# Optimization experiments

Measured on AMD Instinct MI355X. Metric: run time of the kernel, lower is better.

The kernel has to match this reference:

```python
import jax, jax.numpy as jnp
import numpy as np

G = 16          # grid_size
B = 2           # num graphs
SPACING = 1.5   # anchor_spacing
KA = 8          # atom_k_neighbors
KG = 24         # k_neighbors (grid->atom)
CUTOFF = 8.0
T = 16          # n_atom_types
H = 240         # hidden irreps dim (64x0e+32x1o+16x2e)
A = 9           # SH attr dim, lmax=2
C = 32          # code_dim
L = 2           # num_layers
BIG = 1e9

# real spherical harmonics, 'integral' normalization, e3nn component order
C0 = 0.28209479177387814   # 1/(2 sqrt(pi))
C1 = 0.4886025119029199    # sqrt(3/(4 pi))
C2A = 1.0925484305920792   # sqrt(15/(4 pi))
C2B = 0.31539156525252005  # sqrt(5/(16 pi))
C2C = 0.5462742152960396   # sqrt(15/(16 pi))

def _sph(rel, dist):
    u = rel / jnp.maximum(dist, 1e-9)[:, None]
    x, y, z = u[:, 0], u[:, 1], u[:, 2]
    return jnp.stack([
        jnp.full_like(x, C0),
        C1 * y, C1 * z, C1 * x,
        C2A * x * y, C2A * y * z, C2B * (3.0 * z * z - 1.0),
        C2A * z * x, C2C * (x * x - y * y),
    ], axis=-1)


def setup_inputs():
    key = jax.random.key(0)
    ks = jax.random.split(key, 12)
    Na = 1024
    half = G * SPACING / 2.0
    pos = jax.random.uniform(ks[0], (Na, 3), minval=-half, maxval=half, dtype=jnp.float32)
    atom_types = jax.random.randint(ks[1], (Na,), 0, T, dtype=jnp.int32)
    atom_batch = jnp.repeat(jnp.arange(B, dtype=jnp.int32), Na // B)

    def lin(k, shape):
        fan_in = shape[-2]
        return jax.random.normal(k, shape, dtype=jnp.float32) / jnp.sqrt(float(fan_in))

    Din = 2 * H + A
    return dict(
        pos=pos, atom_types=atom_types, atom_batch=atom_batch,
        We=lin(ks[2], (T + A, H)), be=jnp.zeros((H,), jnp.float32),
        Wm1=lin(ks[3], (L, Din, H)), bm1=jnp.zeros((L, H), jnp.float32),
        Wm2=lin(ks[4], (L, H, H)), bm2=jnp.zeros((L, H), jnp.float32),
        Wu1=lin(ks[5], (L, Din, H)), bu1=jnp.zeros((L, H), jnp.float32),
        Wu2=lin(ks[6], (L, H, H)), bu2=jnp.zeros((L, H), jnp.float32),
        Wo1=lin(ks[7], (H, H)), bo1=jnp.zeros((H,), jnp.float32),
        Wo2=lin(ks[8], (H, C)), bo2=jnp.zeros((C,), jnp.float32),
    )


def _forward(pos, atom_types, atom_batch, We, be, Wm1, bm1, Wm2, bm2,
             Wu1, bu1, Wu2, bu2, Wo1, bo1, Wo2, bo2):
    Na = pos.shape[0]
    ng = G ** 3
    Ng = B * ng
    N = Na + Ng

    # anchor grid, centered, spacing SPACING
    ax = (jnp.arange(G, dtype=pos.dtype) - (G - 1) / 2.0) * SPACING
    grid = jnp.stack(jnp.meshgrid(ax, ax, ax, indexing='ij'), -1).reshape(-1, 3)  # [ng,3]
    grid_flat = jnp.tile(grid, (B, 1))                                            # [Ng,3]
    grid_batch = jnp.repeat(jnp.arange(B, dtype=atom_batch.dtype), ng)
    node_pos = jnp.concatenate([pos, grid_flat], 0)                               # [N,3]

    # atom-atom knn_graph (no self loops, per-graph)
    d2 = jnp.sum((pos[:, None] - pos[None]) ** 2, -1)                             # [Na,Na]
    d2 = jnp.where(atom_batch[:, None] == atom_batch[None], d2, BIG)
    d2 = jnp.where(jnp.eye(Na, dtype=bool), BIG, d2)
    _, nbr = jax.lax.top_k(-d2, KA)                                               # [Na,KA]

    # grid->atom knn (per-graph), edge src=atom, dst=grid node
    d2g = jnp.sum((grid_flat[:, None] - pos[None]) ** 2, -1)                      # [Ng,Na]
    d2g = jnp.where(grid_batch[:, None] == atom_batch[None], d2g, BIG)
    _, nbg = jax.lax.top_k(-d2g, KG)                                              # [Ng,KG]

    src = jnp.concatenate([nbr.reshape(-1), nbg.reshape(-1)])
    dst = jnp.concatenate([jnp.repeat(jnp.arange(Na), KA),
                           Na + jnp.repeat(jnp.arange(Ng), KG)])

    rel = node_pos[src] - node_pos[dst]
    dist = jnp.linalg.norm(rel, axis=-1)
    mask = (dist <= CUTOFF).astype(pos.dtype)        # cutoff as mask (jit-friendly)
    ea = _sph(rel, dist) * mask[:, None]             # [E,A]

    # node attrs: scatter-mean of edge SH over destination nodes
    na_sum = jax.ops.segment_sum(ea, dst, num_segments=N)
    cnt = jax.ops.segment_sum(mask, dst, num_segments=N)
    node_attr = na_sum / jnp.maximum(cnt, 1.0)[:, None]
    node_attr = node_attr.at[:, 0].set(1.0)

    # node features: one-hot atoms, zeros for anchors
    feat = jnp.concatenate([jax.nn.one_hot(atom_types, T, dtype=pos.dtype),
                            jnp.zeros((Ng, T), pos.dtype)], 0)
    h = jax.nn.silu(jnp.concatenate([feat, node_attr], -1) @ We + be)

    # SEGNN-style message passing (attr-conditioned MLPs, masked-sum aggregation)
    for l in range(L):
        mi = jnp.concatenate([h[src], h[dst], ea], -1)                            # [E,2H+A]
        m = jax.nn.silu(jax.nn.silu(mi @ Wm1[l] + bm1[l]) @ Wm2[l] + bm2[l])
        m = m * mask[:, None]
        agg = jax.ops.segment_sum(m, dst, num_segments=N)                         # [N,H]
        ui = jnp.concatenate([h, agg, node_attr], -1)                             # [N,2H+A]
        h = h + jax.nn.silu(jax.nn.silu(ui @ Wu1[l] + bu1[l]) @ Wu2[l] + bu2[l])

    out = jax.nn.silu(h @ Wo1 + bo1) @ Wo2 + bo2                                  # [N,C]
    return out[Na:].reshape(B, ng, C)


def reference(pos, atom_types, atom_batch, We, be, Wm1, bm1, Wm2, bm2,
              Wu1, bu1, Wu2, bu2, Wo1, bo1, Wo2, bo2):
    return _forward(pos, atom_types, atom_batch, We, be, Wm1, bm1, Wm2, bm2,
                    Wu1, bu1, Wu2, bu2, Wo1, bo1, Wo2, bo2)
```

## Files before the change

### kernel.cpp

```cpp
#include <hip/hip_runtime.h>
#include <math.h>

#define NA   1024
#define NGRID 4096
#define NB   2
#define NG   (NB*NGRID)
#define NN   (NA+NG)
#define KAK  8
#define KGK  24
#define EAE  (NA*KAK)
#define EGE  (NG*KGK)
#define ET   (EAE+EGE)
#define HD   240
#define TT   16
#define DIN  489
#define CD   32
#define CUTF 8.0f

typedef __attribute__((ext_vector_type(8))) short short8;
typedef __attribute__((ext_vector_type(4))) short short4v;
typedef __attribute__((ext_vector_type(4))) float f32x4;
typedef __attribute__((ext_vector_type(4))) int i32x4;

__device__ __forceinline__ float silu_f(float x) {
    return x / (1.0f + __expf(-x));
}
__device__ __forceinline__ short f2bf(float x) {
    unsigned u = __float_as_uint(x);
    unsigned r = (u + 0x7FFFu + ((u >> 16) & 1u)) >> 16;
    return (short)r;
}
__device__ __forceinline__ float bf2f(short s) {
    return __uint_as_float(((unsigned)(unsigned short)s) << 16);
}
__device__ __forceinline__ unsigned cvt_pk_bf16(float lo, float hi) {
    unsigned r;
    asm("v_cvt_pk_bf16_f32 %0, %1, %2" : "=v"(r) : "v"(lo), "v"(hi));
    return r;
}

template <int K>
__device__ __forceinline__ void wave_topk(unsigned long long key[8], int lane,
                                          int* __restrict__ outp) {
    unsigned long long lmin = key[0];
#pragma unroll
    for (int s = 1; s < 8; ++s) lmin = key[s] < lmin ? key[s] : lmin;
    int myout = -1;
    for (int t = 0; t < K; ++t) {
        unsigned long long m = lmin;
#pragma unroll
        for (int d = 1; d < 64; d <<= 1) {
            unsigned long long o = __shfl_xor(m, d);
            m = o < m ? o : m;
        }
        if (lane == t) myout = (int)(m & 1023u);
        if (m == lmin) {
#pragma unroll
            for (int s = 0; s < 8; ++s) if (key[s] == m) key[s] = ~0ull;
            lmin = key[0];
#pragma unroll
            for (int s = 1; s < 8; ++s) lmin = key[s] < lmin ? key[s] : lmin;
        }
    }
    if (lane < K) outp[lane] = myout;
}

__global__ __launch_bounds__(256) void knn_kernel(const float* __restrict__ pos,
                                                  int* __restrict__ nbr,
                                                  int* __restrict__ nbg) {
    __shared__ float sx[512], sy[512], sz[512];
    int tid = threadIdx.x;
    bool isAtom = blockIdx.x < (NA / 4);
    int q0 = isAtom ? blockIdx.x * 4 : (blockIdx.x - NA / 4) * 4;
    int pbase;
    if (isAtom) pbase = (q0 >= 512) ? 512 : 0;
    else        pbase = (q0 >= NGRID) ? 512 : 0;
    for (int j = tid; j < 512; j += 256) {
        sx[j] = pos[(pbase + j)*3 + 0];
        sy[j] = pos[(pbase + j)*3 + 1];
        sz[j] = pos[(pbase + j)*3 + 2];
    }
    __syncthreads();
    int lane = tid & 63;
    int qq = q0 + (tid >> 6);
    if (isAtom) {
        int i = qq;
        float px = sx[i - pbase], py = sy[i - pbase], pz = sz[i - pbase];
        unsigned long long key[8];
#pragma unroll
        for (int s = 0; s < 8; ++s) {
            int c = s * 64 + lane;
            int j = pbase + c;
            float dx = px - sx[c], dy = py - sy[c], dz = pz - sz[c];
            float d2 = __fadd_rn(__fadd_rn(__fmul_rn(dx,dx), __fmul_rn(dy,dy)), __fmul_rn(dz,dz));
            key[s] = ((unsigned long long)__float_as_uint(d2) << 10) | (unsigned)j;
            if (j == i) key[s] = ~0ull;
        }
        wave_topk<KAK>(key, lane, &nbr[i*KAK]);
    } else {
        int g = qq;
        int gi = g & (NGRID - 1);
        int ix = gi >> 8, iy = (gi >> 4) & 15, iz = gi & 15;
        float px = ((float)ix - 7.5f) * 1.5f;
        float py = ((float)iy - 7.5f) * 1.5f;
        float pz = ((float)iz - 7.5f) * 1.5f;
        unsigned long long key[8];
#pragma unroll
        for (int s = 0; s < 8; ++s) {
            int c = s * 64 + lane;
            int j = pbase + c;
            float dx = px - sx[c], dy = py - sy[c], dz = pz - sz[c];
            float d2 = __fadd_rn(__fadd_rn(__fmul_rn(dx,dx), __fmul_rn(dy,dy)), __fmul_rn(dz,dz));
            key[s] = ((unsigned long long)__float_as_uint(d2) << 10) | (unsigned)j;
        }
        wave_topk<KGK>(key, lane, &nbg[g*KGK]);
    }
}

__global__ void edge_kernel(const float* __restrict__ pos, const int* __restrict__ nbr,
                            const int* __restrict__ nbg, float* __restrict__ ea,
                            float* __restrict__ emask) {
    int e = blockIdx.x * blockDim.x + threadIdx.x;
    if (e >= ET) return;
    int src; float dpx, dpy, dpz;
    if (e < EAE) {
        int d = e >> 3;
        src = nbr[e];
        dpx = pos[d*3]; dpy = pos[d*3+1]; dpz = pos[d*3+2];
    } else {
        int eg = e - EAE;
        src = nbg[eg];
        int gg = eg / KGK;
        int gi = gg % NGRID;
        int ix = gi >> 8, iy = (gi >> 4) & 15, iz = gi & 15;
        dpx = ((float)ix - 7.5f) * 1.5f;
        dpy = ((float)iy - 7.5f) * 1.5f;
        dpz = ((float)iz - 7.5f) * 1.5f;
    }
    float rx = pos[src*3] - dpx, ry = pos[src*3+1] - dpy, rz = pos[src*3+2] - dpz;
    float dist = sqrtf(rx*rx + ry*ry + rz*rz);
    float mask = (dist <= CUTF) ? 1.0f : 0.0f;
    float inv = 1.0f / fmaxf(dist, 1e-9f);
    float x = rx * inv, y = ry * inv, z = rz * inv;
    float s0 = 0.28209479177387814f;
    float s1 = 0.4886025119029199f * y;
    float s2 = 0.4886025119029199f * z;
    float s3 = 0.4886025119029199f * x;
    float s4 = 1.0925484305920792f * x * y;
    float s5 = 1.0925484305920792f * y * z;
    float s6 = 0.31539156525252005f * (3.0f * z * z - 1.0f);
    float s7 = 1.0925484305920792f * z * x;
    float s8 = 0.5462742152960396f * (x * x - y * y);
    float* o = &ea[(size_t)e * 9];
    o[0] = s0 * mask; o[1] = s1 * mask; o[2] = s2 * mask; o[3] = s3 * mask;
    o[4] = s4 * mask; o[5] = s5 * mask; o[6] = s6 * mask; o[7] = s7 * mask; o[8] = s8 * mask;
    emask[e] = mask;
}

__global__ void node_attr_kernel(const float* __restrict__ ea, const float* __restrict__ emask,
                                 float* __restrict__ attr) {
    int n = blockIdx.x * blockDim.x + threadIdx.x;
    if (n >= NN) return;
    int K, e0;
    if (n < NA) { K = KAK; e0 = n * KAK; }
    else        { K = KGK; e0 = EAE + (n - NA) * KGK; }
    float s[9];
#pragma unroll
    for (int a = 0; a < 9; ++a) s[a] = 0.f;
    float cnt = 0.f;
    for (int k = 0; k < K; ++k) {
        cnt += emask[e0 + k];
        const float* p = &ea[(size_t)(e0 + k) * 9];
#pragma unroll
        for (int a = 0; a < 9; ++a) s[a] += p[a];
    }
    float invc = 1.0f / fmaxf(cnt, 1.0f);
    attr[n*9+0] = 1.0f;
#pragma unroll
    for (int a = 1; a < 9; ++a) attr[n*9+a] = s[a] * invc;
}

__global__ void encoder_kernel(const int* __restrict__ types, const float* __restrict__ attr,
                               const float* __restrict__ We, const float* __restrict__ be,
                               float* __restrict__ h) {
    int idx = blockIdx.x * blockDim.x + threadIdx.x;
    int n = idx / HD, j = idx % HD;
    float acc = be[j];
    if (n < NA) acc += We[types[n] * HD + j];
#pragma unroll
    for (int a = 0; a < 9; ++a) acc += attr[n*9+a] * We[(TT + a) * HD + j];
    h[idx] = silu_f(acc);
}

__global__ void convert_all_kernel(const float* __restrict__ Wm2, const float* __restrict__ Wu1,
                                   const float* __restrict__ Wu2, const float* __restrict__ Wm1,
                                   short* __restrict__ wm2t, short* __restrict__ wu1t,
                                   short* __restrict__ wu2t,
                                   short* __restrict__ wzd_hi, short* __restrict__ wzd_lo,
                                   short* __restrict__ wzs_hi, short* __restrict__ wzs_lo) {
    int idx = blockIdx.x * blockDim.x + threadIdx.x;
    if (idx < 131072) {
        int l = idx >> 16, rem = idx & 65535, col = rem >> 8, k = rem & 255;
        short v = 0;
        if (k < 240 && col < 240) v = f2bf(Wm2[(size_t)l*57600 + k*240 + col]);
        wm2t[idx] = v;
    } else if (idx < 393216) {
        int i = idx - 131072;
        int l = i / 131072, rem = i % 131072, col = rem >> 9, k = rem & 511;
        short v = 0;
        if (k < DIN && col < 240) v = f2bf(Wu1[(size_t)l*DIN*240 + (size_t)k*240 + col]);
        wu1t[i] = v;
    } else if (idx < 524288) {
        int i = idx - 393216;
        int l = i >> 16, rem = i & 65535, col = rem >> 8, k = rem & 255;
        short v = 0;
        if (k < 240 && col < 240) v = f2bf(Wu2[(size_t)l*57600 + k*240 + col]);
        wu2t[i] = v;
    } else if (idx < 655360) {
        int i = idx - 524288;
        int l = i >> 16, rem = i & 65535, col = rem >> 8, k = rem & 255;
        float v = 0.f;
        if (k < 240 && col < 240) v = Wm1[(size_t)l*DIN*HD + (size_t)(240 + k)*HD + col];
        short hh = f2bf(v);
        wzd_hi[i] = hh;
        wzd_lo[i] = f2bf(v - bf2f(hh));
    } else {
        int i = idx - 655360;
        int l = i >> 16, rem = i & 65535, col = rem >> 8, k = rem & 255;
        float v = 0.f;
        if (k < 240 && col < 240) v = Wm1[(size_t)l*DIN*HD + (size_t)k*HD + col];
        short hh = f2bf(v);
        wzs_hi[i] = hh;
        wzs_lo[i] = f2bf(v - bf2f(hh));
    }
}

__global__ __launch_bounds__(256) void node_z_mfma_kernel(
        const float* __restrict__ h,
        const short* __restrict__ wzd_hi, const short* __restrict__ wzd_lo,
        const short* __restrict__ wzs_hi, const short* __restrict__ wzs_lo,
        const float* __restrict__ bm1,
        float* __restrict__ Zs, float* __restrict__ Zd) {
    __shared__ __align__(16) short Ahi[32 * 256];
    __shared__ __align__(16) short Alo[32 * 256];
    int tid = threadIdx.x;
    int n0 = blockIdx.x * 32;

#pragma unroll
    for (int it = 0; it < 4; ++it) {
        int idx = it * 256 + tid;
        int row = idx >> 5, q = idx & 31;
        int j = q * 8;
        short8 ohi = {0,0,0,0,0,0,0,0}, olo = {0,0,0,0,0,0,0,0};
        if (j < 240) {
            const float4 a0 = *(const float4*)(h + (size_t)(n0 + row) * HD + j);
            const float4 a1 = *(const float4*)(h + (size_t)(n0 + row) * HD + j + 4);
            float v[8] = {a0.x, a0.y, a0.z, a0.w, a1.x, a1.y, a1.z, a1.w};
#pragma unroll
            for (int a = 0; a < 8; ++a) {
                short hh = f2bf(v[a]);
                ohi[a] = hh;
                olo[a] = f2bf(v[a] - bf2f(hh));
            }
        }
        int boff = row * 512 + ((q * 16) ^ ((row & 7) << 4));
        *(short8*)((char*)Ahi + boff) = ohi;
        *(short8*)((char*)Alo + boff) = olo;
    }
    __syncthreads();

    int wid = tid >> 6, lane = tid & 63;
    int mw = wid >> 1, nw = wid & 1;
    int lg = lane >> 4, lc = lane & 15;
    int col0 = nw * 128;
    int arow = (mw * 16 + lc) * 256;

    f32x4 acc[8];
#pragma unroll
    for (int nt = 0; nt < 8; ++nt) acc[nt] = (f32x4){0.f, 0.f, 0.f, 0.f};
#pragma unroll
    for (int kc = 0; kc < 8; ++kc) {
        int aoff = arow + ((kc * 32 + lg * 8) ^ ((lc & 7) << 3));
        const short8 ahi = *(const short8*)&Ahi[aoff];
        const short8 alo = *(const short8*)&Alo[aoff];
#pragma unroll
        for (int nt = 0; nt < 8; ++nt) {
            size_t bo = (size_t)(col0 + nt*16 + lc) * 256 + kc*32 + lg*8;
            const short8 bhi = *(const short8*)(wzd_hi + bo);
            const short8 blo = *(const short8*)(wzd_lo + bo);
            acc[nt] = __builtin_amdgcn_mfma_f32_16x16x32_bf16(ahi, bhi, acc[nt], 0, 0, 0);
            acc[nt] = __builtin_amdgcn_mfma_f32_16x16x32_bf16(ahi, blo, acc[nt], 0, 0, 0);
            acc[nt] = __builtin_amdgcn_mfma_f32_16x16x32_bf16(alo, bhi, acc[nt], 0, 0, 0);
        }
    }
#pragma unroll
    for (int nt = 0; nt < 8; ++nt) {
        int ncol = col0 + nt * 16 + lc;
        if (ncol < HD) {
            float bias = bm1[ncol];
            float vals[4] = {acc[nt].x, acc[nt].y, acc[nt].z, acc[nt].w};
#pragma unroll
            for (int r = 0; r < 4; ++r)
                Zd[(size_t)(n0 + mw*16 + lg*4 + r) * HD + ncol] = vals[r] + bias;
        }
    }

    if (n0 < NA) {
#pragma unroll
        for (int nt = 0; nt < 8; ++nt) acc[nt] = (f32x4){0.f, 0.f, 0.f, 0.f};
#pragma unroll
        for (int kc = 0; kc < 8; ++kc) {
            int aoff = arow + ((kc * 32 + lg * 8) ^ ((lc & 7) << 3));
            const short8 ahi = *(const short8*)&Ahi[aoff];
            const short8 alo = *(const short8*)&Alo[aoff];
#pragma unroll
            for (int nt = 0; nt < 8; ++nt) {
                size_t bo = (size_t)(col0 + nt*16 + lc) * 256 + kc*32 + lg*8;
                const short8 bhi = *(const short8*)(wzs_hi + bo);
                const short8 blo = *(const short8*)(wzs_lo + bo);
                acc[nt] = __builtin_amdgcn_mfma_f32_16x16x32_bf16(ahi, bhi, acc[nt], 0, 0, 0);
                acc[nt] = __builtin_amdgcn_mfma_f32_16x16x32_bf16(ahi, blo, acc[nt], 0, 0, 0);
                acc[nt] = __builtin_amdgcn_mfma_f32_16x16x32_bf16(alo, bhi, acc[nt], 0, 0, 0);
            }
        }
#pragma unroll
        for (int nt = 0; nt < 8; ++nt) {
            int ncol = col0 + nt * 16 + lc;
            if (ncol < HD) {
                float vals[4] = {acc[nt].x, acc[nt].y, acc[nt].z, acc[nt].w};
#pragma unroll
                for (int r = 0; r < 4; ++r)
                    Zs[(size_t)(n0 + mw*16 + lg*4 + r) * HD + ncol] = vals[r];
            }
        }
    }
}

__global__ __launch_bounds__(256) void msg_gemm_kernel(
        const float* __restrict__ Zs, const float* __restrict__ Zd,
        const int* __restrict__ nbg, const float* __restrict__ ea,
        const float* __restrict__ emask, const float* __restrict__ Wea,
        const short* __restrict__ wm2t, const float* __restrict__ bm2,
        float* __restrict__ agg) {
    __shared__ __align__(16) short Abuf[48 * 256];
    __shared__ __align__(16) float mkbuf[48];
    int tid = threadIdx.x;
    int blk = blockIdx.x;
    int e0 = blk * 48;

    int q = tid & 31;
    int rh = tid >> 5;
    float4 w0[9], w1[9];
    float4 zdA0, zdA1, zdB0, zdB1;
    int srcs[6];
    if (q < 30) {
        int j = q * 8;
#pragma unroll
        for (int a = 0; a < 9; ++a) {
            w0[a] = *(const float4*)(Wea + a * HD + j);
            w1[a] = *(const float4*)(Wea + a * HD + j + 4);
        }
#pragma unroll
        for (int r8 = 0; r8 < 6; ++r8) srcs[r8] = nbg[e0 + rh + r8 * 8];
        int dn0 = NA + blk * 2;
        zdA0 = *(const float4*)(Zd + (size_t)dn0 * HD + j);
        zdA1 = *(const float4*)(Zd + (size_t)dn0 * HD + j + 4);
        zdB0 = *(const float4*)(Zd + (size_t)(dn0 + 1) * HD + j);
        zdB1 = *(const float4*)(Zd + (size_t)(dn0 + 1) * HD + j + 4);
    }
    if (tid < 48) mkbuf[tid] = emask[EAE + e0 + tid];

#pragma unroll
    for (int r8 = 0; r8 < 6; ++r8) {
        int row = rh + r8 * 8;
        i32x4 oi = (i32x4){0, 0, 0, 0};
        if (q < 30) {
            int j = q * 8;
            int eg = e0 + row;
            int srcn = srcs[r8];
            const float4 zs0 = *(const float4*)(Zs + (size_t)srcn * HD + j);
            const float4 zs1 = *(const float4*)(Zs + (size_t)srcn * HD + j + 4);
            const float4 zd0 = (r8 < 3) ? zdA0 : zdB0;
            const float4 zd1 = (r8 < 3) ? zdA1 : zdB1;
            float s0 = zs0.x + zd0.x, s1 = zs0.y + zd0.y, s2 = zs0.z + zd0.z, s3 = zs0.w + zd0.w;
            float s4 = zs1.x + zd1.x, s5 = zs1.y + zd1.y, s6 = zs1.z + zd1.z, s7 = zs1.w + zd1.w;
            const float* ep = ea + (size_t)(EAE + eg) * 9;
#pragma unroll
            for (int a = 0; a < 9; ++a) {
                float e = ep[a];
                s0 += e * w0[a].x; s1 += e * w0[a].y; s2 += e * w0[a].z; s3 += e * w0[a].w;
                s4 += e * w1[a].x; s5 += e * w1[a].y; s6 += e * w1[a].z; s7 += e * w1[a].w;
            }
            oi[0] = (int)cvt_pk_bf16(silu_f(s0), silu_f(s1));
            oi[1] = (int)cvt_pk_bf16(silu_f(s2), silu_f(s3));
            oi[2] = (int)cvt_pk_bf16(silu_f(s4), silu_f(s5));
            oi[3] = (int)cvt_pk_bf16(silu_f(s6), silu_f(s7));
        }
        *(i32x4*)((char*)Abuf + row * 512 + ((q * 16) ^ ((row & 7) << 4))) = oi;
    }
    __syncthreads();

    int wid = tid >> 6, lane = tid & 63;
    int lg = lane >> 4, lc = lane & 15;
    int col0 = wid * 64;

    f32x4 acc[3][4];
#pragma unroll
    for (int mt = 0; mt < 3; ++mt)
#pragma unroll
        for (int nt = 0; nt < 4; ++nt) acc[mt][nt] = (f32x4){0.f, 0.f, 0.f, 0.f};

#pragma unroll
    for (int kc = 0; kc < 8; ++kc) {
        short8 af[3];
#pragma unroll
        for (int mt = 0; mt < 3; ++mt)
            af[mt] = *(const short8*)&Abuf[(mt*16 + lc) * 256 +
                                           ((kc*32 + lg*8) ^ ((lc & 7) << 3))];
#pragma unroll
        for (int nt = 0; nt < 4; ++nt) {
            const short8 bf = *(const short8*)(wm2t + (size_t)(col0 + nt*16 + lc) * 256 + kc*32 + lg*8);
#pragma unroll
            for (int mt = 0; mt < 3; ++mt)
                acc[mt][nt] = __builtin_amdgcn_mfma_f32_16x16x32_bf16(af[mt], bf, acc[mt][nt], 0, 0, 0);
        }
    }

#pragma unroll
    for (int nt = 0; nt < 4; ++nt) {
        int ncol = col0 + nt * 16 + lc;
        float bias = (ncol < HD) ? bm2[ncol] : 0.f;
        float p[3];
#pragma unroll
        for (int mt = 0; mt < 3; ++mt) {
            const float4 mkv = *(const float4*)&mkbuf[mt*16 + lg*4];
            float t0 = silu_f(acc[mt][nt].x + bias) * mkv.x;
            float t1 = silu_f(acc[mt][nt].y + bias) * mkv.y;
            float t2 = silu_f(acc[mt][nt].z + bias) * mkv.z;
            float t3 = silu_f(acc[mt][nt].w + bias) * mkv.w;
            p[mt] = (t0 + t1) + (t2 + t3);
        }
        float v0 = p[0] + ((lg < 2) ? p[1] : 0.f);
        float v1 = ((lg >= 2) ? p[1] : 0.f) + p[2];
        v0 += __shfl_xor(v0, 16); v0 += __shfl_xor(v0, 32);
        v1 += __shfl_xor(v1, 16); v1 += __shfl_xor(v1, 32);
        if (ncol < HD) {
            int node = NA + blk * 2;
            if (lane < 16)      agg[(size_t)(node + 0) * HD + ncol] = v0;
            else if (lane < 32) agg[(size_t)(node + 1) * HD + ncol] = v1;
        }
    }
}

template <int KE, int NPB>
__global__ __launch_bounds__(192) void msg_mfma_kernel(
        const float* __restrict__ Zs, const float* __restrict__ Zd,
        const int* __restrict__ nbrList, const float* __restrict__ ea,
        const float* __restrict__ emask, const float* __restrict__ Wea,
        const short* __restrict__ wm2t, const float* __restrict__ bm2,
        float* __restrict__ agg, int dstBase, int edgeBase) {
    constexpr int ROWS = KE * NPB;
    constexpr int MT = ROWS / 16;
    __shared__ __align__(16) short Abuf[ROWS * 264];
    __shared__ __align__(16) float mkbuf[ROWS];

    int tid = threadIdx.x;
    int b = blockIdx.x;
    int e0 = edgeBase + b * ROWS;

    if (tid < ROWS) mkbuf[tid] = emask[e0 + tid];
    for (int idx = tid; idx < ROWS * 24; idx += 192) {
        int r = idx / 24;
        Abuf[r * 264 + 240 + (idx % 24)] = 0;
    }
    for (int idx = tid; idx < ROWS * 60; idx += 192) {
        int row = idx / 60;
        int j = (idx % 60) * 4;
        int srcn = nbrList[b * ROWS + row];
        int dstn = dstBase + b * NPB + row / KE;
        const float4 zs = *(const float4*)(Zs + (size_t)srcn * HD + j);
        const float4 zd = *(const float4*)(Zd + (size_t)dstn * HD + j);
        float s0 = zs.x + zd.x, s1 = zs.y + zd.y, s2 = zs.z + zd.z, s3 = zs.w + zd.w;
        const float* ep = ea + (size_t)(e0 + row) * 9;
#pragma unroll
        for (int a = 0; a < 9; ++a) {
            float ev = ep[a];
            const float4 w = *(const float4*)(Wea + a * HD + j);
            s0 += ev * w.x; s1 += ev * w.y; s2 += ev * w.z; s3 += ev * w.w;
        }
        short4v o;
        o.x = f2bf(silu_f(s0)); o.y = f2bf(silu_f(s1));
        o.z = f2bf(silu_f(s2)); o.w = f2bf(silu_f(s3));
        *(short4v*)&Abuf[row * 264 + j] = o;
    }
    __syncthreads();

    int w = tid / 64, lane = tid % 64;
    int lg = lane >> 4, lc = lane & 15;
    int wcol0 = w * 80;

    f32x4 acc[MT][5];
#pragma unroll
    for (int mt = 0; mt < MT; ++mt)
#pragma unroll
        for (int nt = 0; nt < 5; ++nt) acc[mt][nt] = (f32x4){0.f, 0.f, 0.f, 0.f};

#pragma unroll
    for (int kc = 0; kc < 8; ++kc) {
        short8 af[MT];
#pragma unroll
        for (int mt = 0; mt < MT; ++mt)
            af[mt] = *(const short8*)&Abuf[(mt * 16 + lc) * 264 + kc * 32 + lg * 8];
#pragma unroll
        for (int nt = 0; nt < 5; ++nt) {
            const short8 bf = *(const short8*)(wm2t + (size_t)(wcol0 + nt * 16 + lc) * 256 + kc * 32 + lg * 8);
#pragma unroll
            for (int mt = 0; mt < MT; ++mt)
                acc[mt][nt] = __builtin_amdgcn_mfma_f32_16x16x32_bf16(af[mt], bf, acc[mt][nt], 0, 0, 0);
        }
    }

#pragma unroll
    for (int nt = 0; nt < 5; ++nt) {
        int ncol = wcol0 + nt * 16 + lc;
        float bias = bm2[ncol];
        float p[MT];
#pragma unroll
        for (int mt = 0; mt < MT; ++mt) {
            const float4 mkv = *(const float4*)&mkbuf[mt * 16 + lg * 4];
            float t0 = silu_f(acc[mt][nt].x + bias) * mkv.x;
            float t1 = silu_f(acc[mt][nt].y + bias) * mkv.y;
            float t2 = silu_f(acc[mt][nt].z + bias) * mkv.z;
            float t3 = silu_f(acc[mt][nt].w + bias) * mkv.w;
            p[mt] = (t0 + t1) + (t2 + t3);
        }
#pragma unroll
        for (int mt = 0; mt < MT; ++mt) {
            float v = p[mt];
            v += __shfl_xor(v, 16);
            if (lane < 16)
                agg[(size_t)(dstBase + b * (2 * MT) + 2 * mt + 0) * HD + ncol] = v;
            else if (lane >= 32 && lane < 48)
                agg[(size_t)(dstBase + b * (2 * MT) + 2 * mt + 1) * HD + ncol] = v;
        }
    }
}

__global__ __launch_bounds__(256) void update_mfma_kernel(
        float* __restrict__ h, const float* __restrict__ agg,
        const float* __restrict__ attr,
        const short* __restrict__ wu1t, const float* __restrict__ bu1,
        const short* __restrict__ wu2t, const float* __restrict__ bu2) {
    __shared__ __align__(16) short Abuf[32 * 512];
    __shared__ __align__(16) short Ubuf[32 * 256];
    int tid = threadIdx.x;
    int n0 = blockIdx.x * 32;

#pragma unroll
    for (int it = 0; it < 8; ++it) {
        int idx = it * 256 + tid;
        int row = idx >> 6, q = idx & 63;
        int j = q * 8;
        int n = n0 + row;
        short8 o = {0,0,0,0,0,0,0,0};
        if (j < 240) {
            const float4 a0 = *(const float4*)(h + (size_t)n * HD + j);
            const float4 a1 = *(const float4*)(h + (size_t)n * HD + j + 4);
            o[0]=f2bf(a0.x); o[1]=f2bf(a0.y); o[2]=f2bf(a0.z); o[3]=f2bf(a0.w);
            o[4]=f2bf(a1.x); o[5]=f2bf(a1.y); o[6]=f2bf(a1.z); o[7]=f2bf(a1.w);
        } else if (j < 480) {
            const float4 a0 = *(const float4*)(agg + (size_t)n * HD + (j - 240));
            const float4 a1 = *(const float4*)(agg + (size_t)n * HD + (j - 240) + 4);
            o[0]=f2bf(a0.x); o[1]=f2bf(a0.y); o[2]=f2bf(a0.z); o[3]=f2bf(a0.w);
            o[4]=f2bf(a1.x); o[5]=f2bf(a1.y); o[6]=f2bf(a1.z); o[7]=f2bf(a1.w);
        } else if (j == 480) {
#pragma unroll
            for (int a = 0; a < 8; ++a) o[a] = f2bf(attr[n*9 + a]);
        } else if (j == 488) {
            o[0] = f2bf(attr[n*9 + 8]);
        }
        *(short8*)((char*)Abuf + row * 1024 + ((q * 16) ^ ((row & 7) << 4))) = o;
    }
    __syncthreads();

    int wid = tid >> 6, lane = tid & 63;
    int mw = wid >> 1, nw = wid & 1;
    int lg = lane >> 4, lc = lane & 15;
    int col0 = nw * 128;

    f32x4 acc[8];
#pragma unroll
    for (int nt = 0; nt < 8; ++nt) acc[nt] = (f32x4){0.f, 0.f, 0.f, 0.f};
#pragma unroll
    for (int kc = 0; kc < 16; ++kc) {
        const short8 af = *(const short8*)((char*)Abuf + (mw*16 + lc) * 1024 +
                                           ((kc*64 + lg*16) ^ ((lc & 7) << 4)));
#pragma unroll
        for (int nt = 0; nt < 8; ++nt) {
            const short8 bf = *(const short8*)(wu1t + (size_t)(col0 + nt*16 + lc) * 512 + kc*32 + lg*8);
            acc[nt] = __builtin_amdgcn_mfma_f32_16x16x32_bf16(af, bf, acc[nt], 0, 0, 0);
        }
    }
#pragma unroll
    for (int nt = 0; nt < 8; ++nt) {
        int ncol = col0 + nt * 16 + lc;
        float bias = (ncol < HD) ? bu1[ncol] : 0.f;
        float vals[4] = {acc[nt].x, acc[nt].y, acc[nt].z, acc[nt].w};
#pragma unroll
        for (int r = 0; r < 4; ++r) {
            int row = mw*16 + lg*4 + r;
            *(short*)((char*)Ubuf + row * 512 + ((ncol * 2) ^ ((row & 7) << 4))) =
                f2bf(silu_f(vals[r] + bias));
        }
    }
    __syncthreads();

    f32x4 acc2[8];
#pragma unroll
    for (int nt = 0; nt < 8; ++nt) acc2[nt] = (f32x4){0.f, 0.f, 0.f, 0.f};
#pragma unroll
    for (int kc = 0; kc < 8; ++kc) {
        const short8 af = *(const short8*)((char*)Ubuf + (mw*16 + lc) * 512 +
                                           ((kc*64 + lg*16) ^ ((lc & 7) << 4)));
#pragma unroll
        for (int nt = 0; nt < 8; ++nt) {
            const short8 bf = *(const short8*)(wu2t + (size_t)(col0 + nt*16 + lc) * 256 + kc*32 + lg*8);
            acc2[nt] = __builtin_amdgcn_mfma_f32_16x16x32_bf16(af, bf, acc2[nt], 0, 0, 0);
        }
    }
#pragma unroll
    for (int nt = 0; nt < 8; ++nt) {
        int ncol = col0 + nt * 16 + lc;
        if (ncol < HD) {
            float bias = bu2[ncol];
            float vals[4] = {acc2[nt].x, acc2[nt].y, acc2[nt].z, acc2[nt].w};
#pragma unroll
            for (int r = 0; r < 4; ++r) {
                int row = mw*16 + lg*4 + r;
                size_t hi = (size_t)(n0 + row) * HD + ncol;
                h[hi] += silu_f(vals[r] + bias);
            }
        }
    }
}

__global__ void output_kernel(const float* __restrict__ h,
                              const float* __restrict__ Wo1, const float* __restrict__ bo1,
                              const float* __restrict__ Wo2, const float* __restrict__ bo2,
                              float* __restrict__ out) {
    const int NBT = 4;
    __shared__ float hr[NBT][HD];
    __shared__ float o1[NBT][HD];
    int tid = threadIdx.x;
    int g0 = blockIdx.x * NBT;
    for (int idx = tid; idx < NBT * HD; idx += 256) {
        int k = idx / HD, i = idx % HD;
        hr[k][i] = h[(size_t)(NA + g0 + k) * HD + i];
    }
    __syncthreads();
    int j = tid;
    if (j < HD) {
        float acc[NBT] = {0.f, 0.f, 0.f, 0.f};
        for (int i4 = 0; i4 < 60; ++i4) {
            int i = 4 * i4;
            float w0 = Wo1[(i+0)*HD+j], w1 = Wo1[(i+1)*HD+j];
            float w2 = Wo1[(i+2)*HD+j], w3 = Wo1[(i+3)*HD+j];
#pragma unroll
            for (int k = 0; k < NBT; ++k) {
                const float4 a = *reinterpret_cast<const float4*>(&hr[k][i]);
                acc[k] += a.x*w0 + a.y*w1 + a.z*w2 + a.w*w3;
            }
        }
        float bb = bo1[j];
#pragma unroll
        for (int k = 0; k < NBT; ++k) o1[k][j] = silu_f(acc[k] + bb);
    }
    __syncthreads();
    if (tid < NBT * CD) {
        int k = tid >> 5, c = tid & 31;
        float acc = bo2[c];
        for (int i = 0; i < HD; ++i) acc += o1[k][i] * Wo2[i*CD + c];
        out[(size_t)(g0 + k) * CD + c] = acc;
    }
}

extern "C" void kernel_launch(void* const* d_in, const int* in_sizes, int n_in,
                              void* d_out, int out_size, void* d_ws, size_t ws_size,
                              hipStream_t stream) {
    (void)in_sizes; (void)n_in; (void)out_size; (void)ws_size;
    const float* pos   = (const float*)d_in[0];
    const int*   types = (const int*)d_in[1];
    const int*   batch = (const int*)d_in[2];
    (void)batch;
    const float* We    = (const float*)d_in[3];
    const float* be    = (const float*)d_in[4];
    const float* Wm1   = (const float*)d_in[5];
    const float* bm1   = (const float*)d_in[6];
    const float* Wm2   = (const float*)d_in[7];
    const float* bm2   = (const float*)d_in[8];
    const float* Wu1   = (const float*)d_in[9];
    const float* bu1   = (const float*)d_in[10];
    const float* Wu2   = (const float*)d_in[11];
    const float* bu2   = (const float*)d_in[12];
    const float* Wo1   = (const float*)d_in[13];
    const float* bo1   = (const float*)d_in[14];
    const float* Wo2   = (const float*)d_in[15];
    const float* bo2   = (const float*)d_in[16];
    float* out = (float*)d_out;

    char* ws = (char*)d_ws;
    size_t off = 0;
    auto take = [&](size_t bytes) -> char* {
        char* p = ws + off;
        off = (off + bytes + 255) & ~(size_t)255;
        return p;
    };
    int*   nbr    = (int*)take((size_t)EAE * 4);
    int*   nbg    = (int*)take((size_t)EGE * 4);
    float* ea     = (float*)take((size_t)ET * 9 * 4);
    float* emask  = (float*)take((size_t)ET * 4);
    float* attr   = (float*)take((size_t)NN * 9 * 4);
    float* h      = (float*)take((size_t)NN * HD * 4);
    float* agg    = (float*)take((size_t)NN * HD * 4);
    float* zs     = (float*)take((size_t)NA * HD * 4);
    float* zd     = (float*)take((size_t)NN * HD * 4);
    short* wm2t   = (short*)take((size_t)2 * 256 * 256 * 2);
    short* wu1t   = (short*)take((size_t)2 * 256 * 512 * 2);
    short* wu2t   = (short*)take((size_t)2 * 256 * 256 * 2);
    short* wzd_hi = (short*)take((size_t)2 * 256 * 256 * 2);
    short* wzd_lo = (short*)take((size_t)2 * 256 * 256 * 2);
    short* wzs_hi = (short*)take((size_t)2 * 256 * 256 * 2);
    short* wzs_lo = (short*)take((size_t)2 * 256 * 256 * 2);

    knn_kernel<<<NA/4 + NG/4, 256, 0, stream>>>(pos, nbr, nbg);
    edge_kernel<<<ET/256, 256, 0, stream>>>(pos, nbr, nbg, ea, emask);
    node_attr_kernel<<<NN/256, 256, 0, stream>>>(ea, emask, attr);
    encoder_kernel<<<(NN*HD)/256, 256, 0, stream>>>(types, attr, We, be, h);
    convert_all_kernel<<<786432/256, 256, 0, stream>>>(Wm2, Wu1, Wu2, Wm1,
                                                       wm2t, wu1t, wu2t,
                                                       wzd_hi, wzd_lo, wzs_hi, wzs_lo);

    for (int l = 0; l < 2; ++l) {
        const float* wm1 = Wm1 + (size_t)l * DIN * HD;
        const float* wea = wm1 + (size_t)480 * HD;
        const short* w2t = wm2t + (size_t)l * 256 * 256;
        const float* bb2 = bm2 + l * HD;
        node_z_mfma_kernel<<<NN/32, 256, 0, stream>>>(
            h,
            wzd_hi + (size_t)l * 65536, wzd_lo + (size_t)l * 65536,
            wzs_hi + (size_t)l * 65536, wzs_lo + (size_t)l * 65536,
            bm1 + l * HD, zs, zd);
        msg_mfma_kernel<KAK, 8><<<NA*KAK/64, 192, 0, stream>>>(
            zs, zd, nbr, ea, emask, wea, w2t, bb2, agg, 0, 0);
        msg_gemm_kernel<<<EGE/48, 256, 0, stream>>>(zs, zd, nbg, ea, emask, wea, w2t, bb2, agg);
        update_mfma_kernel<<<NN/32, 256, 0, stream>>>(
            h, agg, attr,
            wu1t + (size_t)l * 256 * 512, bu1 + l * HD,
            wu2t + (size_t)l * 256 * 256, bu2 + l * HD);
    }
    output_kernel<<<NG/4, 256, 0, stream>>>(h, Wo1, bo1, Wo2, bo2, out);
}
```

Before: 626.0 us.

## Split edge attributes into vector arrays and double-buffer msg_gemm over four tiles

Result: slower. 723.4 us (+15.6%).

```diff
diff --git a/kernel.cpp b/kernel.cpp
--- a/kernel.cpp
+++ b/kernel.cpp
@@ -118,7 +118,8 @@
 }
 
 __global__ void edge_kernel(const float* __restrict__ pos, const int* __restrict__ nbr,
-                            const int* __restrict__ nbg, float* __restrict__ ea,
+                            const int* __restrict__ nbg, float4* __restrict__ eaA,
+                            float4* __restrict__ eaB, float* __restrict__ eaC,
                             float* __restrict__ emask) {
     int e = blockIdx.x * blockDim.x + threadIdx.x;
     if (e >= ET) return;
@@ -151,13 +152,14 @@
     float s6 = 0.31539156525252005f * (3.0f * z * z - 1.0f);
     float s7 = 1.0925484305920792f * z * x;
     float s8 = 0.5462742152960396f * (x * x - y * y);
-    float* o = &ea[(size_t)e * 9];
-    o[0] = s0 * mask; o[1] = s1 * mask; o[2] = s2 * mask; o[3] = s3 * mask;
-    o[4] = s4 * mask; o[5] = s5 * mask; o[6] = s6 * mask; o[7] = s7 * mask; o[8] = s8 * mask;
+    eaA[e] = (float4){s0*mask, s1*mask, s2*mask, s3*mask};
+    eaB[e] = (float4){s4*mask, s5*mask, s6*mask, s7*mask};
+    eaC[e] = s8 * mask;
     emask[e] = mask;
 }
 
-__global__ void node_attr_kernel(const float* __restrict__ ea, const float* __restrict__ emask,
+__global__ void node_attr_kernel(const float4* __restrict__ eaA, const float4* __restrict__ eaB,
+                                 const float* __restrict__ eaC, const float* __restrict__ emask,
                                  float* __restrict__ attr) {
     int n = blockIdx.x * blockDim.x + threadIdx.x;
     if (n >= NN) return;
@@ -170,9 +172,11 @@
     float cnt = 0.f;
     for (int k = 0; k < K; ++k) {
         cnt += emask[e0 + k];
-        const float* p = &ea[(size_t)(e0 + k) * 9];
-#pragma unroll
-        for (int a = 0; a < 9; ++a) s[a] += p[a];
+        const float4 a0 = eaA[e0 + k];
+        const float4 a1 = eaB[e0 + k];
+        s[0] += a0.x; s[1] += a0.y; s[2] += a0.z; s[3] += a0.w;
+        s[4] += a1.x; s[5] += a1.y; s[6] += a1.z; s[7] += a1.w;
+        s[8] += eaC[e0 + k];
     }
     float invc = 1.0f / fmaxf(cnt, 1.0f);
     attr[n*9+0] = 1.0f;
@@ -338,21 +342,20 @@
 
 __global__ __launch_bounds__(256) void msg_gemm_kernel(
         const float* __restrict__ Zs, const float* __restrict__ Zd,
-        const int* __restrict__ nbg, const float* __restrict__ ea,
+        const int* __restrict__ nbg,
+        const float4* __restrict__ eaA, const float4* __restrict__ eaB,
+        const float* __restrict__ eaC,
         const float* __restrict__ emask, const float* __restrict__ Wea,
         const short* __restrict__ wm2t, const float* __restrict__ bm2,
         float* __restrict__ agg) {
-    __shared__ __align__(16) short Abuf[48 * 256];
-    __shared__ __align__(16) float mkbuf[48];
+    __shared__ __align__(16) short Abuf[2][48 * 256];
+    __shared__ __align__(16) float mkbuf[2][48];
     int tid = threadIdx.x;
-    int blk = blockIdx.x;
-    int e0 = blk * 48;
+    int blk0 = blockIdx.x * 4;
 
     int q = tid & 31;
     int rh = tid >> 5;
     float4 w0[9], w1[9];
-    float4 zdA0, zdA1, zdB0, zdB1;
-    int srcs[6];
     if (q < 30) {
         int j = q * 8;
 #pragma unroll
@@ -360,102 +363,127 @@
             w0[a] = *(const float4*)(Wea + a * HD + j);
             w1[a] = *(const float4*)(Wea + a * HD + j + 4);
         }
-#pragma unroll
-        for (int r8 = 0; r8 < 6; ++r8) srcs[r8] = nbg[e0 + rh + r8 * 8];
-        int dn0 = NA + blk * 2;
-        zdA0 = *(const float4*)(Zd + (size_t)dn0 * HD + j);
-        zdA1 = *(const float4*)(Zd + (size_t)dn0 * HD + j + 4);
-        zdB0 = *(const float4*)(Zd + (size_t)(dn0 + 1) * HD + j);
-        zdB1 = *(const float4*)(Zd + (size_t)(dn0 + 1) * HD + j + 4);
-    }
-    if (tid < 48) mkbuf[tid] = emask[EAE + e0 + tid];
-
-#pragma unroll
-    for (int r8 = 0; r8 < 6; ++r8) {
-        int row = rh + r8 * 8;
-        i32x4 oi = (i32x4){0, 0, 0, 0};
+    }
+
+    auto assemble = [&](int tile, int bufi) {
+        int e0 = tile * 48;
+        if (tid < 48) mkbuf[bufi][tid] = emask[EAE + e0 + tid];
         if (q < 30) {
             int j = q * 8;
-            int eg = e0 + row;
-            int srcn = srcs[r8];
-            const float4 zs0 = *(const float4*)(Zs + (size_t)srcn * HD + j);
-            const float4 zs1 = *(const float4*)(Zs + (size_t)srcn * HD + j + 4);
-            const float4 zd0 = (r8 < 3) ? zdA0 : zdB0;
-            const float4 zd1 = (r8 < 3) ? zdA1 : zdB1;
-            float s0 = zs0.x + zd0.x, s1 = zs0.y + zd0.y, s2 = zs0.z + zd0.z, s3 = zs0.w + zd0.w;
-            float s4 = zs1.x + zd1.x, s5 = zs1.y + zd1.y, s6 = zs1.z + zd1.z, s7 = zs1.w + zd1.w;
-            const float* ep = ea + (size_t)(EAE + eg) * 9;
-#pragma unroll
-            for (int a = 0; a < 9; ++a) {
-                float e = ep[a];
-                s0 += e * w0[a].x; s1 += e * w0[a].y; s2 += e * w0[a].z; s3 += e * w0[a].w;
-                s4 += e * w1[a].x; s5 += e * w1[a].y; s6 += e * w1[a].z; s7 += e * w1[a].w;
-            }
-            oi[0] = (int)cvt_pk_bf16(silu_f(s0), silu_f(s1));
-            oi[1] = (int)cvt_pk_bf16(silu_f(s2), silu_f(s3));
-            oi[2] = (int)cvt_pk_bf16(silu_f(s4), silu_f(s5));
-            oi[3] = (int)cvt_pk_bf16(silu_f(s6), silu_f(s7));
-        }
-        *(i32x4*)((char*)Abuf + row * 512 + ((q * 16) ^ ((row & 7) << 4))) = oi;
-    }
+            int srcs[6];
+#pragma unroll
+            for (int r8 = 0; r8 < 6; ++r8) srcs[r8] = nbg[e0 + rh + r8 * 8];
+            int dn0 = NA + tile * 2;
+            const float4 zdA0 = *(const float4*)(Zd + (size_t)dn0 * HD + j);
+            const float4 zdA1 = *(const float4*)(Zd + (size_t)dn0 * HD + j + 4);
+            const float4 zdB0 = *(const float4*)(Zd + (size_t)(dn0 + 1) * HD + j);
+            const float4 zdB1 = *(const float4*)(Zd + (size_t)(dn0 + 1) * HD + j + 4);
+#pragma unroll
+            for (int r8 = 0; r8 < 6; ++r8) {
+                int row = rh + r8 * 8;
+                int eg = e0 + row;
+                int srcn = srcs[r8];
+                const float4 zs0 = *(const float4*)(Zs + (size_t)srcn * HD + j);
+                const float4 zs1 = *(const float4*)(Zs + (size_t)srcn * HD + j + 4);
+                const float4 zd0 = (r8 < 3) ? zdA0 : zdB0;
+                const float4 zd1 = (r8 < 3) ? zdA1 : zdB1;
+                float s0 = zs0.x + zd0.x, s1 = zs0.y + zd0.y, s2 = zs0.z + zd0.z, s3 = zs0.w + zd0.w;
+                float s4 = zs1.x + zd1.x, s5 = zs1.y + zd1.y, s6 = zs1.z + zd1.z, s7 = zs1.w + zd1.w;
+                const float4 ea0 = eaA[EAE + eg];
+                const float4 ea1 = eaB[EAE + eg];
+                const float  ea8 = eaC[EAE + eg];
+                float ev[9] = {ea0.x, ea0.y, ea0.z, ea0.w, ea1.x, ea1.y, ea1.z, ea1.w, ea8};
+#pragma unroll
+                for (int a = 0; a < 9; ++a) {
+                    float e = ev[a];
+                    s0 += e * w0[a].x; s1 += e * w0[a].y; s2 += e * w0[a].z; s3 += e * w0[a].w;
+                    s4 += e * w1[a].x; s5 += e * w1[a].y; s6 += e * w1[a].z; s7 += e * w1[a].w;
+                }
+                i32x4 oi;
+                oi[0] = (int)cvt_pk_bf16(silu_f(s0), silu_f(s1));
+                oi[1] = (int)cvt_pk_bf16(silu_f(s2), silu_f(s3));
+                oi[2] = (int)cvt_pk_bf16(silu_f(s4), silu_f(s5));
+                oi[3] = (int)cvt_pk_bf16(silu_f(s6), silu_f(s7));
+                *(i32x4*)((char*)&Abuf[bufi][0] + row * 512 + ((q * 16) ^ ((row & 7) << 4))) = oi;
+            }
+        } else {
+#pragma unroll
+            for (int r8 = 0; r8 < 6; ++r8) {
+                int row = rh + r8 * 8;
+                i32x4 z = (i32x4){0, 0, 0, 0};
+                *(i32x4*)((char*)&Abuf[bufi][0] + row * 512 + ((q * 16) ^ ((row & 7) << 4))) = z;
+            }
+        }
+    };
+
+    assemble(blk0, 0);
     __syncthreads();
 
     int wid = tid >> 6, lane = tid & 63;
     int lg = lane >> 4, lc = lane & 15;
     int col0 = wid * 64;
 
-    f32x4 acc[3][4];
-#pragma unroll
-    for (int mt = 0; mt < 3; ++mt)
-#pragma unroll
-        for (int nt = 0; nt < 4; ++nt) acc[mt][nt] = (f32x4){0.f, 0.f, 0.f, 0.f};
-
-#pragma unroll
-    for (int kc = 0; kc < 8; ++kc) {
-        short8 af[3];
+#pragma unroll
+    for (int t = 0; t < 4; ++t) {
+        if (t < 3) assemble(blk0 + t + 1, (t + 1) & 1);
+
+        const short* Ab = &Abuf[t & 1][0];
+        f32x4 acc[3][4];
 #pragma unroll
         for (int mt = 0; mt < 3; ++mt)
-            af[mt] = *(const short8*)&Abuf[(mt*16 + lc) * 256 +
-                                           ((kc*32 + lg*8) ^ ((lc & 7) << 3))];
+#pragma unroll
+            for (int nt = 0; nt < 4; ++nt) acc[mt][nt] = (f32x4){0.f, 0.f, 0.f, 0.f};
+
+#pragma unroll
+        for (int kc = 0; kc < 8; ++kc) {
+            short8 af[3];
+#pragma unroll
+            for (int mt = 0; mt < 3; ++mt)
+                af[mt] = *(const short8*)&Ab[(mt*16 + lc) * 256 +
+                                             ((kc*32 + lg*8) ^ ((lc & 7) << 3))];
+#pragma unroll
+            for (int nt = 0; nt < 4; ++nt) {
+                const short8 bf = *(const short8*)(wm2t + (size_t)(col0 + nt*16 + lc) * 256 + kc*32 + lg*8);
+#pragma unroll
+                for (int mt = 0; mt < 3; ++mt)
+                    acc[mt][nt] = __builtin_amdgcn_mfma_f32_16x16x32_bf16(af[mt], bf, acc[mt][nt], 0, 0, 0);
+            }
+        }
+
 #pragma unroll
         for (int nt = 0; nt < 4; ++nt) {
-            const short8 bf = *(const short8*)(wm2t + (size_t)(col0 + nt*16 + lc) * 256 + kc*32 + lg*8);
-#pragma unroll
-            for (int mt = 0; mt < 3; ++mt)
-                acc[mt][nt] = __builtin_amdgcn_mfma_f32_16x16x32_bf16(af[mt], bf, acc[mt][nt], 0, 0, 0);
-        }
-    }
-
-#pragma unroll
-    for (int nt = 0; nt < 4; ++nt) {
-        int ncol = col0 + nt * 16 + lc;
-        float bias = (ncol < HD) ? bm2[ncol] : 0.f;
-        float p[3];
-#pragma unroll
-        for (int mt = 0; mt < 3; ++mt) {
-            const float4 mkv = *(const float4*)&mkbuf[mt*16 + lg*4];
-            float t0 = silu_f(acc[mt][nt].x + bias) * mkv.x;
-            float t1 = silu_f(acc[mt][nt].y + bias) * mkv.y;
-            float t2 = silu_f(acc[mt][nt].z + bias) * mkv.z;
-            float t3 = silu_f(acc[mt][nt].w + bias) * mkv.w;
-            p[mt] = (t0 + t1) + (t2 + t3);
-        }
-        float v0 = p[0] + ((lg < 2) ? p[1] : 0.f);
-        float v1 = ((lg >= 2) ? p[1] : 0.f) + p[2];
-        v0 += __shfl_xor(v0, 16); v0 += __shfl_xor(v0, 32);
-        v1 += __shfl_xor(v1, 16); v1 += __shfl_xor(v1, 32);
-        if (ncol < HD) {
-            int node = NA + blk * 2;
-            if (lane < 16)      agg[(size_t)(node + 0) * HD + ncol] = v0;
-            else if (lane < 32) agg[(size_t)(node + 1) * HD + ncol] = v1;
-        }
+            int ncol = col0 + nt * 16 + lc;
+            float bias = (ncol < HD) ? bm2[ncol] : 0.f;
+            float p[3];
+#pragma unroll
+            for (int mt = 0; mt < 3; ++mt) {
+                const float4 mkv = *(const float4*)&mkbuf[t & 1][mt*16 + lg*4];
+                float t0 = silu_f(acc[mt][nt].x + bias) * mkv.x;
+                float t1 = silu_f(acc[mt][nt].y + bias) * mkv.y;
+                float t2 = silu_f(acc[mt][nt].z + bias) * mkv.z;
+                float t3 = silu_f(acc[mt][nt].w + bias) * mkv.w;
+                p[mt] = (t0 + t1) + (t2 + t3);
+            }
+            float v0 = p[0] + ((lg < 2) ? p[1] : 0.f);
+            float v1 = ((lg >= 2) ? p[1] : 0.f) + p[2];
+            v0 += __shfl_xor(v0, 16); v0 += __shfl_xor(v0, 32);
+            v1 += __shfl_xor(v1, 16); v1 += __shfl_xor(v1, 32);
+            if (ncol < HD) {
+                int node = NA + (blk0 + t) * 2;
+                if (lane < 16)      agg[(size_t)(node + 0) * HD + ncol] = v0;
+                else if (lane < 32) agg[(size_t)(node + 1) * HD + ncol] = v1;
+            }
+        }
+        __syncthreads();
     }
 }
 
 template <int KE, int NPB>
 __global__ __launch_bounds__(192) void msg_mfma_kernel(
         const float* __restrict__ Zs, const float* __restrict__ Zd,
-        const int* __restrict__ nbrList, const float* __restrict__ ea,
+        const int* __restrict__ nbrList,
+        const float4* __restrict__ eaA, const float4* __restrict__ eaB,
+        const float* __restrict__ eaC,
         const float* __restrict__ emask, const float* __restrict__ Wea,
         const short* __restrict__ wm2t, const float* __restrict__ bm2,
         float* __restrict__ agg, int dstBase, int edgeBase) {
@@ -481,12 +509,15 @@
         const float4 zs = *(const float4*)(Zs + (size_t)srcn * HD + j);
         const float4 zd = *(const float4*)(Zd + (size_t)dstn * HD + j);
         float s0 = zs.x + zd.x, s1 = zs.y + zd.y, s2 = zs.z + zd.z, s3 = zs.w + zd.w;
-        const float* ep = ea + (size_t)(e0 + row) * 9;
+        const float4 ea0 = eaA[e0 + row];
+        const float4 ea1 = eaB[e0 + row];
+        const float  ea8 = eaC[e0 + row];
+        float ev[9] = {ea0.x, ea0.y, ea0.z, ea0.w, ea1.x, ea1.y, ea1.z, ea1.w, ea8};
 #pragma unroll
         for (int a = 0; a < 9; ++a) {
-            float ev = ep[a];
+            float e = ev[a];
             const float4 w = *(const float4*)(Wea + a * HD + j);
-            s0 += ev * w.x; s1 += ev * w.y; s2 += ev * w.z; s3 += ev * w.w;
+            s0 += e * w.x; s1 += e * w.y; s2 += e * w.z; s3 += e * w.w;
         }
         short4v o;
         o.x = f2bf(silu_f(s0)); o.y = f2bf(silu_f(s1));
@@ -715,26 +746,28 @@
         off = (off + bytes + 255) & ~(size_t)255;
         return p;
     };
-    int*   nbr    = (int*)take((size_t)EAE * 4);
-    int*   nbg    = (int*)take((size_t)EGE * 4);
-    float* ea     = (float*)take((size_t)ET * 9 * 4);
-    float* emask  = (float*)take((size_t)ET * 4);
-    float* attr   = (float*)take((size_t)NN * 9 * 4);
-    float* h      = (float*)take((size_t)NN * HD * 4);
-    float* agg    = (float*)take((size_t)NN * HD * 4);
-    float* zs     = (float*)take((size_t)NA * HD * 4);
-    float* zd     = (float*)take((size_t)NN * HD * 4);
-    short* wm2t   = (short*)take((size_t)2 * 256 * 256 * 2);
-    short* wu1t   = (short*)take((size_t)2 * 256 * 512 * 2);
-    short* wu2t   = (short*)take((size_t)2 * 256 * 256 * 2);
-    short* wzd_hi = (short*)take((size_t)2 * 256 * 256 * 2);
-    short* wzd_lo = (short*)take((size_t)2 * 256 * 256 * 2);
-    short* wzs_hi = (short*)take((size_t)2 * 256 * 256 * 2);
-    short* wzs_lo = (short*)take((size_t)2 * 256 * 256 * 2);
+    int*    nbr    = (int*)take((size_t)EAE * 4);
+    int*    nbg    = (int*)take((size_t)EGE * 4);
+    float4* eaA    = (float4*)take((size_t)ET * 16);
+    float4* eaB    = (float4*)take((size_t)ET * 16);
+    float*  eaC    = (float*)take((size_t)ET * 4);
+    float*  emask  = (float*)take((size_t)ET * 4);
+    float*  attr   = (float*)take((size_t)NN * 9 * 4);
+    float*  h      = (float*)take((size_t)NN * HD * 4);
+    float*  agg    = (float*)take((size_t)NN * HD * 4);
+    float*  zs     = (float*)take((size_t)NA * HD * 4);
+    float*  zd     = (float*)take((size_t)NN * HD * 4);
+    short*  wm2t   = (short*)take((size_t)2 * 256 * 256 * 2);
+    short*  wu1t   = (short*)take((size_t)2 * 256 * 512 * 2);
+    short*  wu2t   = (short*)take((size_t)2 * 256 * 256 * 2);
+    short*  wzd_hi = (short*)take((size_t)2 * 256 * 256 * 2);
+    short*  wzd_lo = (short*)take((size_t)2 * 256 * 256 * 2);
+    short*  wzs_hi = (short*)take((size_t)2 * 256 * 256 * 2);
+    short*  wzs_lo = (short*)take((size_t)2 * 256 * 256 * 2);
 
     knn_kernel<<<NA/4 + NG/4, 256, 0, stream>>>(pos, nbr, nbg);
-    edge_kernel<<<ET/256, 256, 0, stream>>>(pos, nbr, nbg, ea, emask);
-    node_attr_kernel<<<NN/256, 256, 0, stream>>>(ea, emask, attr);
+    edge_kernel<<<ET/256, 256, 0, stream>>>(pos, nbr, nbg, eaA, eaB, eaC, emask);
+    node_attr_kernel<<<NN/256, 256, 0, stream>>>(eaA, eaB, eaC, emask, attr);
     encoder_kernel<<<(NN*HD)/256, 256, 0, stream>>>(types, attr, We, be, h);
     convert_all_kernel<<<786432/256, 256, 0, stream>>>(Wm2, Wu1, Wu2, Wm1,
                                                        wm2t, wu1t, wu2t,
@@ -751,8 +784,9 @@
             wzs_hi + (size_t)l * 65536, wzs_lo + (size_t)l * 65536,
             bm1 + l * HD, zs, zd);
         msg_mfma_kernel<KAK, 8><<<NA*KAK/64, 192, 0, stream>>>(
-            zs, zd, nbr, ea, emask, wea, w2t, bb2, agg, 0, 0);
-        msg_gemm_kernel<<<EGE/48, 256, 0, stream>>>(zs, zd, nbg, ea, emask, wea, w2t, bb2, agg);
+            zs, zd, nbr, eaA, eaB, eaC, emask, wea, w2t, bb2, agg, 0, 0);
+        msg_gemm_kernel<<<EGE/192, 256, 0, stream>>>(zs, zd, nbg, eaA, eaB, eaC,
+                                                     emask, wea, w2t, bb2, agg);
         update_mfma_kernel<<<NN/32, 256, 0, stream>>>(
             h, agg, attr,
             wu1t + (size_t)l * 256 * 512, bu1 + l * HD,
```
